# Kernel optimization log

Measured on AMD Instinct MI355X. Metric: run time of the kernel, lower is better.

The kernel has to match this reference:

```python
import jax, jax.numpy as jnp
import numpy as np

N_NODES = 100000
N_EDGES = 600000
N_GRAPHS = 64
EPS = 1e-5


def setup_inputs() -> dict:
    key = jax.random.key(0)
    ks = jax.random.split(key, 8)
    x = jax.random.normal(ks[0], (N_NODES, 128), dtype=jnp.float32)
    edge_index = jax.random.randint(ks[1], (2, N_EDGES), 0, N_NODES, dtype=jnp.int64)
    batch = jnp.sort(jax.random.randint(ks[2], (N_NODES,), 0, N_GRAPHS, dtype=jnp.int64))
    conv_w = jax.random.normal(ks[3], (6, 128, 128), dtype=jnp.float32) * (1.0 / np.sqrt(128))
    conv_b = jnp.zeros((6, 128), dtype=jnp.float32)
    bn_g = jnp.ones((6, 128), dtype=jnp.float32)
    bn_b = jnp.zeros((6, 128), dtype=jnp.float32)
    lin1_w = jax.random.normal(ks[4], (128, 64), dtype=jnp.float32) * (1.0 / np.sqrt(128))
    lin1_b = jnp.zeros((64,), dtype=jnp.float32)
    lin2_w = jax.random.normal(ks[5], (64, 4), dtype=jnp.float32) * (1.0 / np.sqrt(64))
    lin2_b = jnp.zeros((4,), dtype=jnp.float32)
    return {"x": x, "edge_index": edge_index, "batch": batch,
            "conv_w": conv_w, "conv_b": conv_b, "bn_g": bn_g, "bn_b": bn_b,
            "lin1_w": lin1_w, "lin1_b": lin1_b, "lin2_w": lin2_w, "lin2_b": lin2_b}


def reference(x, edge_index, batch, conv_w, conv_b, bn_g, bn_b, lin1_w, lin1_b, lin2_w, lin2_b):
    src, dst = edge_index[0], edge_index[1]  # messages flow src -> dst (PyG source_to_target)
    n = x.shape[0]
    h = x
    # 6 stacked GCNConv(normalize=False) -> ReLU -> BatchNorm1d (training-mode batch stats)
    for i in range(6):
        m = h @ conv_w[i]                                   # [N, H] transform first
        agg = jax.ops.segment_sum(m[src], dst, num_segments=n) + conv_b[i]
        h = jax.nn.relu(agg)
        mean = h.mean(axis=0)
        var = h.var(axis=0)                                  # biased, matches torch BN
        h = (h - mean) * jax.lax.rsqrt(var + EPS) * bn_g[i] + bn_b[i]
    # global mean pool over graphs
    s = jax.ops.segment_sum(h, batch, num_segments=N_GRAPHS)          # [G, H]
    cnt = jax.ops.segment_sum(jnp.ones((n,), h.dtype), batch, num_segments=N_GRAPHS)
    pooled = s / jnp.maximum(cnt, 1.0)[:, None]
    out = pooled @ lin1_w + lin1_b
    out = out @ lin2_w + lin2_b
    return jax.nn.log_softmax(out, axis=-1)
```

## Files before the change

kernel.cpp:

```cpp
#include <hip/hip_runtime.h>
#include <math.h>

#define NN 100000
#define NE 600000
#define NG 64
#define HD 128
#define NL 6
#define NB 1563
#define PSL 16

typedef unsigned short ushort_t;
typedef short short8 __attribute__((ext_vector_type(8)));
typedef float floatx4 __attribute__((ext_vector_type(4)));

__device__ __forceinline__ float bf2f(ushort_t u) {
    return __uint_as_float(((unsigned)u) << 16);
}
__device__ __forceinline__ ushort_t f2bf(float f) {
    unsigned u = __float_as_uint(f);
    unsigned r = (u + 0x7fffu + ((u >> 16) & 1u)) >> 16;
    return (ushort_t)r;
}


__global__ __launch_bounds__(256) void k_cast(const float* __restrict__ x,
                                              ushort_t* __restrict__ xb) {
    int i = blockIdx.x * 256 + threadIdx.x;
    if (i < NN * 32) {
        float4 v = ((const float4*)x)[i];
        ((ushort4*)xb)[i] = make_ushort4(f2bf(v.x), f2bf(v.y), f2bf(v.z), f2bf(v.w));
    }
}


__global__ __launch_bounds__(256) void k_wcast(const float* __restrict__ W,
                                               ushort_t* __restrict__ Wt) {
    const float* Wl = W + blockIdx.x * 16384;
    ushort_t* Wtl = Wt + blockIdx.x * 16384;
    for (int id = threadIdx.x; id < 16384; id += 256) {
        int k = id >> 7, c = id & 127;
        Wtl[c * 128 + k] = f2bf(Wl[id]);
    }
}


__global__ __launch_bounds__(256) void k_hist(const int* __restrict__ ei, int* __restrict__ counts) {
    int e = blockIdx.x * 256 + threadIdx.x;
    if (e < NE) atomicAdd(&counts[ei[NE + e]], 1);
}

__global__ __launch_bounds__(256) void k_scan1(const int* __restrict__ counts, int* __restrict__ bsums) {
    __shared__ int s[256];
    int i = blockIdx.x * 256 + threadIdx.x;
    s[threadIdx.x] = (i < NN) ? counts[i] : 0;
    __syncthreads();
    for (int off = 128; off > 0; off >>= 1) {
        if (threadIdx.x < off) s[threadIdx.x] += s[threadIdx.x + off];
        __syncthreads();
    }
    if (threadIdx.x == 0) bsums[blockIdx.x] = s[0];
}

__global__ __launch_bounds__(512) void k_scan2(int* __restrict__ bsums, int nb) {
    __shared__ int s[512];
    int t = threadIdx.x;
    s[t] = (t < nb) ? bsums[t] : 0;
    __syncthreads();
    for (int off = 1; off < 512; off <<= 1) {
        int v = (t >= off) ? s[t - off] : 0;
        __syncthreads();
        s[t] += v;
        __syncthreads();
    }
    if (t < nb) bsums[t] = (t == 0) ? 0 : s[t - 1];
}

__global__ __launch_bounds__(256) void k_scan3(const int* __restrict__ counts, const int* __restrict__ bsums,
                                               int* __restrict__ rowptr) {
    __shared__ int s[256];
    int t = threadIdx.x;
    int i = blockIdx.x * 256 + t;
    int v = (i < NN) ? counts[i] : 0;
    s[t] = v;
    __syncthreads();
    for (int off = 1; off < 256; off <<= 1) {
        int u = (t >= off) ? s[t - off] : 0;
        __syncthreads();
        s[t] += u;
        __syncthreads();
    }
    if (i < NN) rowptr[i] = bsums[blockIdx.x] + s[t] - v;
    if (i == 0) rowptr[NN] = NE;
}

__global__ __launch_bounds__(256) void k_fill(const int* __restrict__ ei, const int* __restrict__ rowptr,
                                              int* __restrict__ cursor, int* __restrict__ colsrc) {
    int e = blockIdx.x * 256 + threadIdx.x;
    if (e < NE) {
        int d = ei[NE + e];
        int pos = rowptr[d] + atomicAdd(&cursor[d], 1);
        colsrc[pos] = ei[e];
    }
}


__global__ __launch_bounds__(256) void k_gconv(
    const ushort_t* __restrict__ hin,
    const int* __restrict__ rowptr, const int* __restrict__ colsrc,
    const float* __restrict__ stats, const float* __restrict__ bng,
    const float* __restrict__ bnb,
    const ushort_t* __restrict__ Wt, const float* __restrict__ bias,
    ushort_t* __restrict__ hout, float* __restrict__ partials) {
    __shared__ float sstat[256];
    int t = threadIdx.x;
    sstat[t] = 0.f;
    int wave = t >> 6, lane = t & 63;
    int l15 = lane & 15, quad = lane >> 4;
    int rowbase = blockIdx.x * 64 + wave * 16;
    int row = rowbase + l15;
    bool valid = row < NN;
    int beg = valid ? rowptr[row] : 0;
    int end = valid ? rowptr[row + 1] : 0;
    int deg = end - beg;
    int maxd = deg;
    maxd = max(maxd, __shfl_xor(maxd, 1, 64));
    maxd = max(maxd, __shfl_xor(maxd, 2, 64));
    maxd = max(maxd, __shfl_xor(maxd, 4, 64));
    maxd = max(maxd, __shfl_xor(maxd, 8, 64));

    float ac[4][8];
    #pragma unroll
    for (int s = 0; s < 4; ++s)
        #pragma unroll
        for (int j = 0; j < 8; ++j) ac[s][j] = 0.f;

    const ushort_t* hbase = hin + quad * 8;
    int e = 0;
    for (; e + 1 < maxd; e += 2) {
        bool on0 = e < deg, on1 = e + 1 < deg;
        int i0 = on0 ? beg + e : 0;
        int i1 = on1 ? beg + e + 1 : 0;
        int s0 = colsrc[i0];
        int s1 = colsrc[i1];
        float m0 = on0 ? 1.f : 0.f;
        float m1 = on1 ? 1.f : 0.f;
        const short8* h0 = (const short8*)(hbase + (size_t)s0 * 128);
        const short8* h1 = (const short8*)(hbase + (size_t)s1 * 128);
        short8 v0[4], v1[4];
        #pragma unroll
        for (int s = 0; s < 4; ++s) { v0[s] = h0[s * 4]; v1[s] = h1[s * 4]; }
        #pragma unroll
        for (int s = 0; s < 4; ++s)
            #pragma unroll
            for (int j = 0; j < 8; ++j) {
                ac[s][j] = fmaf(m0, bf2f((ushort_t)v0[s][j]), ac[s][j]);
                ac[s][j] = fmaf(m1, bf2f((ushort_t)v1[s][j]), ac[s][j]);
            }
    }
    if (e < maxd) {
        bool on0 = e < deg;
        int i0 = on0 ? beg + e : 0;
        int s0 = colsrc[i0];
        float m0 = on0 ? 1.f : 0.f;
        const short8* h0 = (const short8*)(hbase + (size_t)s0 * 128);
        #pragma unroll
        for (int s = 0; s < 4; ++s) {
            short8 v0 = h0[s * 4];
            #pragma unroll
            for (int j = 0; j < 8; ++j)
                ac[s][j] = fmaf(m0, bf2f((ushort_t)v0[j]), ac[s][j]);
        }
    }

    float degf = (float)deg;
    short8 afrag[4];
    #pragma unroll
    for (int s = 0; s < 4; ++s) {
        short8 av;
        #pragma unroll
        for (int j = 0; j < 8; ++j) {
            int f = s * 32 + quad * 8 + j;
            float val;
            if (stats != nullptr) {
                const float inv_n = 1.0f / (float)NN;
                float m = stats[f] * inv_n;
                float var = fmaf(-m, m, stats[HD + f] * inv_n);
                float sc = bng[f] * rsqrtf(var + 1e-5f);
                float sh = bnb[f] - m * sc;
                val = fmaf(sc, ac[s][j], degf * sh);
            } else {
                val = ac[s][j];
            }
            av[j] = (short)f2bf(val);
        }
        afrag[s] = av;
    }

    floatx4 acc[8];
    #pragma unroll
    for (int c = 0; c < 8; ++c) acc[c] = (floatx4){0.f, 0.f, 0.f, 0.f};
    #pragma unroll
    for (int c = 0; c < 8; ++c) {
        size_t boff = (size_t)(16 * c + l15) * 128 + quad * 8;
        #pragma unroll
        for (int s = 0; s < 4; ++s) {
            short8 bf = *(const short8*)(Wt + boff + 32 * s);
            acc[c] = __builtin_amdgcn_mfma_f32_16x16x32_bf16(afrag[s], bf, acc[c], 0, 0, 0);
        }
    }

    __syncthreads();
    int orow0 = rowbase + quad * 4;
    #pragma unroll
    for (int c = 0; c < 8; ++c) {
        int col = 16 * c + l15;
        float bv = bias[col];
        float ls = 0.f, lq = 0.f;
        #pragma unroll
        for (int i = 0; i < 4; ++i) {
            int r = orow0 + i;
            if (r < NN) {
                float v = fmaxf(acc[c][i] + bv, 0.f);
                ushort_t bb = f2bf(v);
                hout[(size_t)r * 128 + col] = bb;
                float vr = bf2f(bb);
                ls += vr;
                lq = fmaf(vr, vr, lq);
            }
        }
        ls += __shfl_xor(ls, 16, 64);
        ls += __shfl_xor(ls, 32, 64);
        lq += __shfl_xor(lq, 16, 64);
        lq += __shfl_xor(lq, 32, 64);
        if (quad == 0) {
            atomicAdd(&sstat[col], ls);
            atomicAdd(&sstat[128 + col], lq);
        }
    }
    __syncthreads();
    partials[(size_t)blockIdx.x * 256 + t] = sstat[t];
}


__global__ __launch_bounds__(256) void k_red(const float* __restrict__ partials,
                                             float* __restrict__ stats) {
    int t = threadIdx.x;
    float s = 0.f;
    for (int r = blockIdx.x; r < NB; r += 64) s += partials[(size_t)r * 256 + t];
    atomicAdd(&stats[t], s);
}


__device__ __forceinline__ int lowerb(const int* __restrict__ b, int n, int key) {
    int lo = 0, hi = n;
    while (lo < hi) {
        int mid = (lo + hi) >> 1;
        if (b[mid] < key) lo = mid + 1;
        else hi = mid;
    }
    return lo;
}

__global__ __launch_bounds__(256) void k_pool1(
    const ushort_t* __restrict__ h, const int* __restrict__ batch,
    float* __restrict__ ppart) {
    int g = blockIdx.x >> 4;
    int sl = blockIdx.x & (PSL - 1);
    int lo = lowerb(batch, NN, g);
    int hi = lowerb(batch, NN, g + 1);
    int cnt = hi - lo;
    int a = lo + (int)(((long long)cnt * sl) >> 4);
    int b = lo + (int)(((long long)cnt * (sl + 1)) >> 4);
    int wave = threadIdx.x >> 6, lane = threadIdx.x & 63;
    const ushort2* h2 = (const ushort2*)h;
    float ax = 0.f, ay = 0.f;
    for (int n = a + wave; n < b; n += 4) {
        ushort2 v = h2[(size_t)n * 64 + lane];
        ax += bf2f(v.x);
        ay += bf2f(v.y);
    }
    __shared__ float2 red[4][64];
    red[wave][lane] = make_float2(ax, ay);
    __syncthreads();
    if (wave == 0) {
        float sx = 0.f, sy = 0.f;
        for (int w = 0; w < 4; ++w) {
            sx += red[w][lane].x;
            sy += red[w][lane].y;
        }
        ((float2*)ppart)[(size_t)blockIdx.x * 64 + lane] = make_float2(sx, sy);
    }
}


__global__ __launch_bounds__(64) void k_pool2(
    const float* __restrict__ ppart, const int* __restrict__ batch,
    const float* __restrict__ stats, const float* __restrict__ bng, const float* __restrict__ bnb,
    float* __restrict__ pooled) {
    int g = blockIdx.x;
    int lane = threadIdx.x;
    float sx = 0.f, sy = 0.f;
    #pragma unroll
    for (int s = 0; s < PSL; ++s) {
        float2 v = ((const float2*)ppart)[(size_t)(g * PSL + s) * 64 + lane];
        sx += v.x;
        sy += v.y;
    }
    int cnt = lowerb(batch, NN, g + 1) - lowerb(batch, NN, g);
    int c0 = lane * 2;
    const float inv_n = 1.0f / (float)NN;
    float m0 = stats[c0] * inv_n, m1 = stats[c0 + 1] * inv_n;
    float var0 = fmaf(-m0, m0, stats[HD + c0] * inv_n);
    float var1 = fmaf(-m1, m1, stats[HD + c0 + 1] * inv_n);
    float sc0 = bng[c0] * rsqrtf(var0 + 1e-5f);
    float sc1 = bng[c0 + 1] * rsqrtf(var1 + 1e-5f);
    float sh0 = bnb[c0] - m0 * sc0;
    float sh1 = bnb[c0 + 1] - m1 * sc1;
    float denom = fmaxf((float)cnt, 1.f);
    float2 o;
    o.x = (sc0 * sx + (float)cnt * sh0) / denom;
    o.y = (sc1 * sy + (float)cnt * sh1) / denom;
    ((float2*)pooled)[g * 64 + lane] = o;
}


__global__ __launch_bounds__(64) void k_head(
    const float* __restrict__ pooled, const float* __restrict__ w1, const float* __restrict__ b1,
    const float* __restrict__ w2, const float* __restrict__ b2, float* __restrict__ out) {
    int g = blockIdx.x;
    int j = threadIdx.x;
    float hid = b1[j];
    const float* p = pooled + g * 128;
    #pragma unroll 8
    for (int k = 0; k < 128; ++k) hid = fmaf(p[k], w1[k * 64 + j], hid);
    float o[4];
    #pragma unroll
    for (int c = 0; c < 4; ++c) {
        float v = hid * w2[j * 4 + c];
        #pragma unroll
        for (int off = 1; off < 64; off <<= 1) v += __shfl_xor(v, off, 64);
        o[c] = v + b2[c];
    }
    if (j == 0) {
        float mx = fmaxf(fmaxf(o[0], o[1]), fmaxf(o[2], o[3]));
        float se = expf(o[0] - mx) + expf(o[1] - mx) + expf(o[2] - mx) + expf(o[3] - mx);
        float ls = mx + logf(se);
        #pragma unroll
        for (int c = 0; c < 4; ++c) out[g * 4 + c] = o[c] - ls;
    }
}

extern "C" void kernel_launch(void* const* d_in, const int* in_sizes, int n_in,
                              void* d_out, int out_size, void* d_ws, size_t ws_size,
                              hipStream_t stream) {
    const float* x = (const float*)d_in[0];
    const int* ei = (const int*)d_in[1];
    const int* batch = (const int*)d_in[2];
    const float* conv_w = (const float*)d_in[3];
    const float* conv_b = (const float*)d_in[4];
    const float* bn_g = (const float*)d_in[5];
    const float* bn_b = (const float*)d_in[6];
    const float* l1w = (const float*)d_in[7];
    const float* l1b = (const float*)d_in[8];
    const float* l2w = (const float*)d_in[9];
    const float* l2b = (const float*)d_in[10];
    float* out = (float*)d_out;
    (void)in_sizes; (void)n_in; (void)out_size; (void)ws_size;

    char* ws = (char*)d_ws;
    int* counts = (int*)(ws + 0);
    int* cursor = (int*)(ws + 400000);
    float* stats = (float*)(ws + 800000);
    const size_t zero_bytes = 806144;
    int* rowptr = (int*)(ws + 806144);
    int* bsums = (int*)(ws + 1206400);
    int* colsrc = (int*)(ws + 1208192);
    float* pooled = (float*)(ws + 3608192);
    float* ppart = (float*)(ws + 3641344);
    float* partials = (float*)(ws + 4165632);
    ushort_t* xb = (ushort_t*)(ws + 5766656);
    ushort_t* hb0 = (ushort_t*)(ws + 31366656);
    ushort_t* hb1 = (ushort_t*)(ws + 56966656);
    ushort_t* wtbuf = (ushort_t*)(ws + 82566656);

    hipMemsetAsync(ws, 0, zero_bytes, stream);

    k_cast<<<(NN * 32 + 255) / 256, 256, 0, stream>>>(x, xb);
    k_wcast<<<NL, 256, 0, stream>>>(conv_w, wtbuf);

    int ebl = (NE + 255) / 256;
    int nb1 = (NN + 255) / 256;
    k_hist<<<ebl, 256, 0, stream>>>(ei, counts);
    k_scan1<<<nb1, 256, 0, stream>>>(counts, bsums);
    k_scan2<<<1, 512, 0, stream>>>(bsums, nb1);
    k_scan3<<<nb1, 256, 0, stream>>>(counts, bsums, rowptr);
    k_fill<<<ebl, 256, 0, stream>>>(ei, rowptr, cursor, colsrc);

    ushort_t* hb[2] = {hb0, hb1};
    for (int L = 0; L < NL; ++L) {
        const ushort_t* hin = (L == 0) ? xb : hb[(L + 1) & 1];
        ushort_t* hout = hb[L & 1];
        const float* lstats = (L == 0) ? nullptr : (stats + (L - 1) * 256);
        const float* lg = (L == 0) ? nullptr : (bn_g + (L - 1) * 128);
        const float* lb = (L == 0) ? nullptr : (bn_b + (L - 1) * 128);
        k_gconv<<<NB, 256, 0, stream>>>(hin, rowptr, colsrc, lstats, lg, lb,
                                        wtbuf + L * 16384, conv_b + L * 128,
                                        hout, partials);
        k_red<<<64, 256, 0, stream>>>(partials, stats + L * 256);
    }
    k_pool1<<<NG * PSL, 256, 0, stream>>>(hb1, batch, ppart);
    k_pool2<<<NG, 64, 0, stream>>>(ppart, batch, stats + 5 * 256, bn_g + 5 * 128, bn_b + 5 * 128, pooled);
    k_head<<<NG, 64, 0, stream>>>(pooled, l1w, l1b, l2w, l2b, out);
}
```

Measured before the change: 786.1 us.

## Sort nodes by in-degree so each 16-row MFMA tile has uniform degree

Adds a counting sort of destination nodes by in-degree (histogram, descending-order scan, fill) that builds a permutation. The graph-conv kernel then processes rows in permuted order, so the 16 rows sharing a wave's gather loop have similar degree and less time is lost waiting on the highest-degree row. Output rows are scattered back through the permutation, which loses write locality. The sort also adds three small kernels and a memset, and it reuses the counts and cursor workspace regions once they are no longer needed.

```diff
diff --git a/kernel.cpp b/kernel.cpp
--- a/kernel.cpp
+++ b/kernel.cpp
@@ -104,8 +104,53 @@
 }
 
 
+__global__ __launch_bounds__(256) void k_dhist(const int* __restrict__ rowptr,
+                                               int* __restrict__ dcount) {
+    __shared__ int lc[64];
+    int t = threadIdx.x;
+    if (t < 64) lc[t] = 0;
+    __syncthreads();
+    int n = blockIdx.x * 256 + t;
+    if (n < NN) {
+        int d = rowptr[n + 1] - rowptr[n];
+        atomicAdd(&lc[min(d, 63)], 1);
+    }
+    __syncthreads();
+    if (t < 64 && lc[t] > 0) atomicAdd(&dcount[t], lc[t]);
+}
+
+__global__ __launch_bounds__(64) void k_dscan(const int* __restrict__ dcount,
+                                              int* __restrict__ doff) {
+    int t = threadIdx.x;
+    int s = 0;
+    for (int b = t + 1; b < 64; ++b) s += dcount[b];
+    doff[t] = s;
+}
+
+__global__ __launch_bounds__(256) void k_dfill(const int* __restrict__ rowptr,
+                                               const int* __restrict__ doff,
+                                               int* __restrict__ dcursor,
+                                               int* __restrict__ perm) {
+    __shared__ int lc[64], lbase[64];
+    int t = threadIdx.x;
+    if (t < 64) lc[t] = 0;
+    __syncthreads();
+    int n = blockIdx.x * 256 + t;
+    int b = 0, my = 0;
+    if (n < NN) {
+        int d = rowptr[n + 1] - rowptr[n];
+        b = min(d, 63);
+        my = atomicAdd(&lc[b], 1);
+    }
+    __syncthreads();
+    if (t < 64 && lc[t] > 0) lbase[t] = atomicAdd(&dcursor[t], lc[t]);
+    __syncthreads();
+    if (n < NN) perm[doff[b] + lbase[b] + my] = n;
+}
+
+
 __global__ __launch_bounds__(256) void k_gconv(
-    const ushort_t* __restrict__ hin,
+    const ushort_t* __restrict__ hin, const int* __restrict__ perm,
     const int* __restrict__ rowptr, const int* __restrict__ colsrc,
     const float* __restrict__ stats, const float* __restrict__ bng,
     const float* __restrict__ bnb,
@@ -117,8 +162,9 @@
     int wave = t >> 6, lane = t & 63;
     int l15 = lane & 15, quad = lane >> 4;
     int rowbase = blockIdx.x * 64 + wave * 16;
-    int row = rowbase + l15;
-    bool valid = row < NN;
+    int idx = rowbase + l15;
+    bool valid = idx < NN;
+    int row = valid ? perm[idx] : 0;
     int beg = valid ? rowptr[row] : 0;
     int end = valid ? rowptr[row + 1] : 0;
     int deg = end - beg;
@@ -209,6 +255,10 @@
         }
     }
 
+    int prow[4];
+    #pragma unroll
+    for (int i = 0; i < 4; ++i) prow[i] = __shfl(row, quad * 4 + i, 64);
+
     __syncthreads();
     int orow0 = rowbase + quad * 4;
     #pragma unroll
@@ -218,11 +268,10 @@
         float ls = 0.f, lq = 0.f;
         #pragma unroll
         for (int i = 0; i < 4; ++i) {
-            int r = orow0 + i;
-            if (r < NN) {
+            if (orow0 + i < NN) {
                 float v = fmaxf(acc[c][i] + bv, 0.f);
                 ushort_t bb = f2bf(v);
-                hout[(size_t)r * 128 + col] = bb;
+                hout[(size_t)prow[i] * 128 + col] = bb;
                 float vr = bf2f(bb);
                 ls += vr;
                 lq = fmaf(vr, vr, lq);
@@ -369,7 +418,11 @@
 
     char* ws = (char*)d_ws;
     int* counts = (int*)(ws + 0);
+    int* dcount = (int*)(ws + 0);
+    int* dcursor = (int*)(ws + 256);
+    int* doff = (int*)(ws + 512);
     int* cursor = (int*)(ws + 400000);
+    int* perm = (int*)(ws + 400000);
     float* stats = (float*)(ws + 800000);
     const size_t zero_bytes = 806144;
     int* rowptr = (int*)(ws + 806144);
@@ -396,6 +449,11 @@
     k_scan3<<<nb1, 256, 0, stream>>>(counts, bsums, rowptr);
     k_fill<<<ebl, 256, 0, stream>>>(ei, rowptr, cursor, colsrc);
 
+    hipMemsetAsync(ws, 0, 512, stream);
+    k_dhist<<<nb1, 256, 0, stream>>>(rowptr, dcount);
+    k_dscan<<<1, 64, 0, stream>>>(dcount, doff);
+    k_dfill<<<nb1, 256, 0, stream>>>(rowptr, doff, dcursor, perm);
+
     ushort_t* hb[2] = {hb0, hb1};
     for (int L = 0; L < NL; ++L) {
         const ushort_t* hin = (L == 0) ? xb : hb[(L + 1) & 1];
@@ -403,7 +461,7 @@
         const float* lstats = (L == 0) ? nullptr : (stats + (L - 1) * 256);
         const float* lg = (L == 0) ? nullptr : (bn_g + (L - 1) * 128);
         const float* lb = (L == 0) ? nullptr : (bn_b + (L - 1) * 128);
-        k_gconv<<<NB, 256, 0, stream>>>(hin, rowptr, colsrc, lstats, lg, lb,
+        k_gconv<<<NB, 256, 0, stream>>>(hin, perm, rowptr, colsrc, lstats, lg, lb,
                                         wtbuf + L * 16384, conv_b + L * 128,
                                         hout, partials);
         k_red<<<64, 256, 0, stream>>>(partials, stats + L * 256);
```

Measured after the change: 762.8 us. 1.03x faster.
